# Performance work log

Measured on AMD Instinct MI355X. Metric: run time of the kernel, lower is better.

Reference implementation:

```python
import jax, jax.numpy as jnp
import numpy as np

HEADS = 16

def setup_inputs() -> dict:
    key = jax.random.key(0)
    ks = jax.random.split(key, 8)
    S, B, D = 2048, 2, 1024
    scale = 0.02
    return {
        'query': jax.random.normal(ks[0], (S, B, D), jnp.float32),
        'key':   jax.random.normal(ks[1], (S, B, D), jnp.float32),
        'value': jax.random.normal(ks[2], (S, B, D), jnp.float32),
        'Wq': jax.random.normal(ks[3], (D, D), jnp.float32) * scale,
        'bq': jnp.zeros((D,), jnp.float32),
        'Wk': jax.random.normal(ks[4], (D, D), jnp.float32) * scale,
        'bk': jnp.zeros((D,), jnp.float32),
        'Wv': jax.random.normal(ks[5], (D, D), jnp.float32) * scale,
        'bv': jnp.zeros((D,), jnp.float32),
        'Wo': jax.random.normal(ks[6], (D, D), jnp.float32) * scale,
        'bo': jnp.zeros((D,), jnp.float32),
    }

def reference(query, key, value, Wq, bq, Wk, bk, Wv, bv, Wo, bo):
    S, B, D = query.shape
    h = HEADS
    dk = D // h
    # projections: nn.Linear stores weight [out, in] -> x @ W.T + b
    q = (query @ Wq.T + bq).reshape(S, B, h, dk)
    k = (key   @ Wk.T + bk).reshape(S, B, h, dk)
    v = (value @ Wv.T + bv).reshape(S, B, h, dk)
    # scores: [i, j, b, h]
    scores = jnp.einsum('ibhd,jbhd->ijbh', q, k) / jnp.sqrt(jnp.asarray(dk, q.dtype))
    # original uses nn.Softmax(dim=1) -> softmax over key axis j
    attn = jax.nn.softmax(scores, axis=1)
    x = jnp.einsum('ijbh,jbhd->ibhd', attn, v).reshape(S, B, D)
    return x @ Wo.T + bo
```

## Files before the change

kernel.cpp:

```cpp
#include <hip/hip_runtime.h>
#include <hip/hip_bf16.h>
#include <math.h>

#define S_LEN  2048
#define NBATCH 2
#define DMODEL 1024
#define NHEADS 16
#define HDIM   64
#define MROWS  (S_LEN*NBATCH)
#define NBH    (NBATCH*NHEADS)

typedef __attribute__((ext_vector_type(8))) short          bf16x8;
typedef __attribute__((ext_vector_type(4))) float          f32x4;
typedef __attribute__((ext_vector_type(8))) unsigned short u16x8;

__device__ __forceinline__ unsigned short f2bf(float x) {
    union { __hip_bfloat16 h; unsigned short u; } c;
    c.h = __float2bfloat16(x);
    return c.u;
}
__device__ __forceinline__ unsigned int pk2(float a, float b) {
    return (unsigned int)f2bf(a) | ((unsigned int)f2bf(b) << 16);
}

__global__ __launch_bounds__(256)
void cvt7(const float* __restrict__ s0, const float* __restrict__ s1,
          const float* __restrict__ s2, const float* __restrict__ s3,
          const float* __restrict__ s4, const float* __restrict__ s5,
          const float* __restrict__ s6,
          unsigned short* __restrict__ d0, unsigned short* __restrict__ d1,
          unsigned short* __restrict__ d2, unsigned short* __restrict__ d3,
          unsigned short* __restrict__ d4, unsigned short* __restrict__ d5,
          unsigned short* __restrict__ d6)
{
    const float* s; unsigned short* d; int n;
    switch (blockIdx.y) {
        case 0: s = s0; d = d0; n = MROWS*DMODEL;  break;
        case 1: s = s1; d = d1; n = MROWS*DMODEL;  break;
        case 2: s = s2; d = d2; n = MROWS*DMODEL;  break;
        case 3: s = s3; d = d3; n = DMODEL*DMODEL; break;
        case 4: s = s4; d = d4; n = DMODEL*DMODEL; break;
        case 5: s = s5; d = d5; n = DMODEL*DMODEL; break;
        default: s = s6; d = d6; n = DMODEL*DMODEL; break;
    }
    int i = (blockIdx.x*256 + threadIdx.x) * 8;
    if (i >= n) return;
    float4 a = *(const float4*)(s + i);
    float4 b = *(const float4*)(s + i + 4);
    u16x8 o;
    o[0] = f2bf(a.x); o[1] = f2bf(a.y); o[2] = f2bf(a.z); o[3] = f2bf(a.w);
    o[4] = f2bf(b.x); o[5] = f2bf(b.y); o[6] = f2bf(b.z); o[7] = f2bf(b.w);
    *(u16x8*)(d + i) = o;
}

#define GBM 128
#define GBN 128
#define GBK 32

__device__ __forceinline__ void gemm_bf16_core(
    const unsigned short* __restrict__ A,
    const unsigned short* __restrict__ W,
    const float* __restrict__ bias,
    float* __restrict__ Cf, unsigned short* __restrict__ Cb,
    int mode, float scale)
{
    __shared__ __align__(16) unsigned short As[GBM*GBK];
    __shared__ __align__(16) unsigned short Bs[GBN*GBK];

    const int tid = threadIdx.x;
    const int l   = tid & 63;
    const int w   = tid >> 6;
    const int m0  = blockIdx.y * GBM;
    const int n0  = blockIdx.x * GBN;
    const int wm  = (w >> 1) * 64;
    const int wn  = (w & 1) * 64;

    f32x4 acc[4][4];
    #pragma unroll
    for (int i = 0; i < 4; ++i)
        #pragma unroll
        for (int j = 0; j < 4; ++j)
            acc[i][j] = (f32x4){0.f, 0.f, 0.f, 0.f};

    const int srow = l >> 2;
    const int scol = (l & 3) * 8;

    for (int k0 = 0; k0 < DMODEL; k0 += GBK) {
        #pragma unroll
        for (int i = 0; i < 2; ++i) {
            int c = w*2 + i;
            const unsigned short* ga = A + (size_t)(m0 + c*16 + srow)*DMODEL + k0 + scol;
            const unsigned short* gb = W + (size_t)(n0 + c*16 + srow)*DMODEL + k0 + scol;
            __builtin_amdgcn_global_load_lds(
                (const __attribute__((address_space(1))) void*)ga,
                (__attribute__((address_space(3))) void*)(As + c*512), 16, 0, 0);
            __builtin_amdgcn_global_load_lds(
                (const __attribute__((address_space(1))) void*)gb,
                (__attribute__((address_space(3))) void*)(Bs + c*512), 16, 0, 0);
        }
        __syncthreads();

        bf16x8 af[4], bfr[4];
        #pragma unroll
        for (int f = 0; f < 4; ++f) {
            af[f]  = *(const bf16x8*)(As + (wm + f*16 + (l & 15))*GBK + (l >> 4)*8);
            bfr[f] = *(const bf16x8*)(Bs + (wn + f*16 + (l & 15))*GBK + (l >> 4)*8);
        }
        #pragma unroll
        for (int i = 0; i < 4; ++i)
            #pragma unroll
            for (int j = 0; j < 4; ++j)
                acc[i][j] = __builtin_amdgcn_mfma_f32_16x16x32_bf16(af[i], bfr[j], acc[i][j], 0, 0, 0);
        __syncthreads();
    }

    const int col_l = l & 15;
    const int row_l = (l >> 4) * 4;
    #pragma unroll
    for (int j = 0; j < 4; ++j) {
        int col = n0 + wn + j*16 + col_l;
        float bv = bias[col];
        #pragma unroll
        for (int i = 0; i < 4; ++i) {
            int mbase = m0 + wm + i*16 + row_l;
            #pragma unroll
            for (int r = 0; r < 4; ++r) {
                int m = mbase + r;
                float vout = (acc[i][j][r] + bv) * scale;
                if (mode == 0) {
                    Cf[(size_t)m*DMODEL + col] = vout;
                } else {
                    int s = m >> 1, b = m & 1;
                    int h = col >> 6, d = col & 63;
                    if (mode == 1)
                        Cb[((size_t)(b*NHEADS + h)*S_LEN + s)*HDIM + d] = f2bf(vout);
                    else
                        Cb[((size_t)(b*NHEADS + h)*HDIM + d)*S_LEN + s] = f2bf(vout);
                }
            }
        }
    }
}

__global__ __launch_bounds__(256)
void gemm_qkv_bf16(const unsigned short* __restrict__ qb, const unsigned short* __restrict__ kb,
                   const unsigned short* __restrict__ vb,
                   const unsigned short* __restrict__ Wqb, const float* __restrict__ bq,
                   const unsigned short* __restrict__ Wkb, const float* __restrict__ bk,
                   const unsigned short* __restrict__ Wvb, const float* __restrict__ bv,
                   unsigned short* __restrict__ qp, unsigned short* __restrict__ kp,
                   unsigned short* __restrict__ vt)
{
    const int z = blockIdx.z;
    const unsigned short* A = (z==0) ? qb  : (z==1) ? kb  : vb;
    const unsigned short* W = (z==0) ? Wqb : (z==1) ? Wkb : Wvb;
    const float* bias       = (z==0) ? bq  : (z==1) ? bk  : bv;
    unsigned short* C       = (z==0) ? qp  : (z==1) ? kp  : vt;
    int   mode  = (z==2) ? 2 : 1;
    float scale = (z==0) ? 0.125f : 1.0f;
    gemm_bf16_core(A, W, bias, nullptr, C, mode, scale);
}

__global__ __launch_bounds__(256)
void gemm_out_bf16(const unsigned short* __restrict__ A, const unsigned short* __restrict__ W,
                   const float* __restrict__ bias, float* __restrict__ C)
{
    gemm_bf16_core(A, W, bias, C, nullptr, 0, 1.0f);
}

#define QBLK  128
#define KVBLK 64

__global__ __launch_bounds__(256)
void attn_mfma(const unsigned short* __restrict__ qp, const unsigned short* __restrict__ kp,
               const unsigned short* __restrict__ vt, unsigned short* __restrict__ x)
{
    __shared__ __align__(16) unsigned short Ks[KVBLK*HDIM];
    __shared__ __align__(16) unsigned short Vs[HDIM*KVBLK];
    __shared__ __align__(16) unsigned short Ps[4][32*KVBLK];

    const int tid = threadIdx.x;
    const int w   = tid >> 6;
    const int l   = tid & 63;
    const int g   = l >> 4;
    const int s16 = l & 15;
    const int q0  = blockIdx.x * QBLK;
    const int bh  = blockIdx.y;
    const int b   = bh >> 4;
    const int h   = bh & 15;
    const size_t base = (size_t)bh * S_LEN * HDIM;

    char* KsB = (char*)Ks;
    char* VsB = (char*)Vs;
    char* PsB = (char*)&Ps[w][0];

    bf16x8 qf[2][2];
    #pragma unroll
    for (int ni = 0; ni < 2; ++ni)
        #pragma unroll
        for (int ks = 0; ks < 2; ++ks) {
            int qrow = q0 + w*32 + ni*16 + s16;
            qf[ni][ks] = *(const bf16x8*)(qp + base + (size_t)qrow*HDIM + ks*32 + g*8);
        }

    f32x4 oacc[2][4];
    #pragma unroll
    for (int ni = 0; ni < 2; ++ni)
        #pragma unroll
        for (int nj = 0; nj < 4; ++nj)
            oacc[ni][nj] = (f32x4){0.f, 0.f, 0.f, 0.f};
    float run_m[2] = {-1e30f, -1e30f};
    float run_l[2] = {0.f, 0.f};

    for (int kt = 0; kt < S_LEN; kt += KVBLK) {
        #pragma unroll
        for (int it = 0; it < 2; ++it) {
            int idx  = it*256 + tid;
            int row  = idx >> 3;
            int u    = (idx & 7) ^ (row & 7);
            const unsigned short* gk = kp + base + (size_t)(kt + row)*HDIM + u*8;
            __builtin_amdgcn_global_load_lds(
                (const __attribute__((address_space(1))) void*)gk,
                (__attribute__((address_space(3))) void*)(Ks + (it*256 + w*64)*8), 16, 0, 0);
            const unsigned short* gv = vt + base + (size_t)row*S_LEN + kt + u*8;
            __builtin_amdgcn_global_load_lds(
                (const __attribute__((address_space(1))) void*)gv,
                (__attribute__((address_space(3))) void*)(Vs + (it*256 + w*64)*8), 16, 0, 0);
        }
        __syncthreads();

        f32x4 sacc[4][2];
        #pragma unroll
        for (int mi = 0; mi < 4; ++mi)
            #pragma unroll
            for (int ni = 0; ni < 2; ++ni)
                sacc[mi][ni] = (f32x4){0.f, 0.f, 0.f, 0.f};

        #pragma unroll
        for (int ks = 0; ks < 2; ++ks) {
            bf16x8 af[4];
            #pragma unroll
            for (int mi = 0; mi < 4; ++mi) {
                int key  = mi*16 + s16;
                int addr = ((key << 7) + (ks << 6) + (g << 4)) ^ ((key & 7) << 4);
                af[mi] = *(const bf16x8*)(KsB + addr);
            }
            #pragma unroll
            for (int mi = 0; mi < 4; ++mi)
                #pragma unroll
                for (int ni = 0; ni < 2; ++ni)
                    sacc[mi][ni] = __builtin_amdgcn_mfma_f32_16x16x32_bf16(
                        af[mi], qf[ni][ks], sacc[mi][ni], 0, 0, 0);
        }

        float al[2];
        #pragma unroll
        for (int ni = 0; ni < 2; ++ni) {
            float tm = -1e30f;
            #pragma unroll
            for (int mi = 0; mi < 4; ++mi)
                #pragma unroll
                for (int r = 0; r < 4; ++r)
                    tm = fmaxf(tm, sacc[mi][ni][r]);
            tm = fmaxf(tm, __shfl_xor(tm, 16));
            tm = fmaxf(tm, __shfl_xor(tm, 32));
            float mn = fmaxf(run_m[ni], tm);
            al[ni] = __expf(run_m[ni] - mn);
            float ps = 0.f;
            int row = ni*16 + s16;
            #pragma unroll
            for (int mi = 0; mi < 4; ++mi) {
                float p0 = __expf(sacc[mi][ni][0] - mn);
                float p1 = __expf(sacc[mi][ni][1] - mn);
                float p2 = __expf(sacc[mi][ni][2] - mn);
                float p3 = __expf(sacc[mi][ni][3] - mn);
                ps += (p0 + p1) + (p2 + p3);
                uint2 wv; wv.x = pk2(p0, p1); wv.y = pk2(p2, p3);
                int addr = ((row << 7) + (mi << 5) + (g << 3)) ^ ((row & 7) << 4);
                *(uint2*)(PsB + addr) = wv;
            }
            ps += __shfl_xor(ps, 16);
            ps += __shfl_xor(ps, 32);
            run_l[ni] = run_l[ni]*al[ni] + ps;
            run_m[ni] = mn;
        }

        float alo[2][4];
        #pragma unroll
        for (int ni = 0; ni < 2; ++ni)
            #pragma unroll
            for (int r = 0; r < 4; ++r)
                alo[ni][r] = __shfl(al[ni], 20*g + r);
        #pragma unroll
        for (int ni = 0; ni < 2; ++ni)
            #pragma unroll
            for (int nj = 0; nj < 4; ++nj)
                #pragma unroll
                for (int r = 0; r < 4; ++r)
                    oacc[ni][nj][r] *= alo[ni][r];

        #pragma unroll
        for (int ks = 0; ks < 2; ++ks) {
            bf16x8 pa[2];
            #pragma unroll
            for (int ni = 0; ni < 2; ++ni) {
                int row  = ni*16 + s16;
                int addr = ((row << 7) + (ks << 6) + (g << 4)) ^ ((row & 7) << 4);
                pa[ni] = *(const bf16x8*)(PsB + addr);
            }
            bf16x8 bv[4];
            #pragma unroll
            for (int nj = 0; nj < 4; ++nj) {
                int d    = nj*16 + s16;
                int addr = ((d << 7) + (ks << 6) + (g << 4)) ^ ((d & 7) << 4);
                bv[nj] = *(const bf16x8*)(VsB + addr);
            }
            #pragma unroll
            for (int ni = 0; ni < 2; ++ni)
                #pragma unroll
                for (int nj = 0; nj < 4; ++nj)
                    oacc[ni][nj] = __builtin_amdgcn_mfma_f32_16x16x32_bf16(
                        pa[ni], bv[nj], oacc[ni][nj], 0, 0, 0);
        }
        __syncthreads();
    }

    #pragma unroll
    for (int ni = 0; ni < 2; ++ni) {
        #pragma unroll
        for (int r = 0; r < 4; ++r) {
            float rl  = __shfl(run_l[ni], 20*g + r);
            float inv = 1.f / rl;
            int row = q0 + w*32 + ni*16 + 4*g + r;
            #pragma unroll
            for (int nj = 0; nj < 4; ++nj) {
                int col = h*HDIM + nj*16 + s16;
                x[(size_t)(row*NBATCH + b)*DMODEL + col] = f2bf(oacc[ni][nj][r] * inv);
            }
        }
    }
}

extern "C" void kernel_launch(void* const* d_in, const int* in_sizes, int n_in,
                              void* d_out, int out_size, void* d_ws, size_t ws_size,
                              hipStream_t stream)
{
    const float* query = (const float*)d_in[0];
    const float* key_i = (const float*)d_in[1];
    const float* value = (const float*)d_in[2];
    const float* Wq = (const float*)d_in[3];
    const float* bq = (const float*)d_in[4];
    const float* Wk = (const float*)d_in[5];
    const float* bk = (const float*)d_in[6];
    const float* Wv = (const float*)d_in[7];
    const float* bv = (const float*)d_in[8];
    const float* Wo = (const float*)d_in[9];
    const float* bo = (const float*)d_in[10];
    float* out = (float*)d_out;

    char* ws = (char*)d_ws;
    unsigned short* qb  = (unsigned short*)(ws);
    unsigned short* kb2 = (unsigned short*)(ws + (size_t) 8*1024*1024);
    unsigned short* vb  = (unsigned short*)(ws + (size_t)16*1024*1024);
    unsigned short* Wqb = (unsigned short*)(ws + (size_t)24*1024*1024);
    unsigned short* Wkb = (unsigned short*)(ws + (size_t)26*1024*1024);
    unsigned short* Wvb = (unsigned short*)(ws + (size_t)28*1024*1024);
    unsigned short* Wob = (unsigned short*)(ws + (size_t)30*1024*1024);
    unsigned short* qp  = (unsigned short*)(ws + (size_t)32*1024*1024);
    unsigned short* kp  = (unsigned short*)(ws + (size_t)40*1024*1024);
    unsigned short* vt  = (unsigned short*)(ws + (size_t)48*1024*1024);
    unsigned short* xab = (unsigned short*)(ws + (size_t)56*1024*1024);

    dim3 gCvt(MROWS*DMODEL/(256*8), 7);
    cvt7<<<gCvt, 256, 0, stream>>>(query, key_i, value, Wq, Wk, Wv, Wo,
                                   qb, kb2, vb, Wqb, Wkb, Wvb, Wob);

    dim3 gProj(DMODEL/GBN, MROWS/GBM, 3);
    gemm_qkv_bf16<<<gProj, 256, 0, stream>>>(qb, kb2, vb,
                                             Wqb, bq, Wkb, bk, Wvb, bv,
                                             qp, kp, vt);

    dim3 gAttn(S_LEN/QBLK, NBH);
    attn_mfma<<<gAttn, 256, 0, stream>>>(qp, kp, vt, xab);

    dim3 gOut(DMODEL/GBN, MROWS/GBM, 1);
    gemm_out_bf16<<<gOut, 256, 0, stream>>>(xab, Wob, bo, out);
}
```

Before: 259.6 us.

## Double-buffer attention KV tiles, exp2 softmax with deferred rescale, tiled V transpose

Attention now runs 512 threads with 16 query rows per wave. It double-buffers the K/V tiles so global-to-LDS loads overlap compute, and removes the trailing barrier. Softmax moves to exp2 with log2e folded into the Q scale, and it skips the running-max rescale when the new max stays within a threshold. The V projection writes its transposed output through an LDS tile as coalesced vector stores, and the output GEMM uses 64-wide N tiles for more blocks. The deferred rescale risks larger intermediate exponent values, and the bigger blocks raise LDS and register pressure.

Result: no change. 261.6 us (+0.7%).

```diff
diff --git a/kernel.cpp b/kernel.cpp
--- a/kernel.cpp
+++ b/kernel.cpp
@@ -9,6 +9,9 @@
 #define HDIM   64
 #define MROWS  (S_LEN*NBATCH)
 #define NBH    (NBATCH*NHEADS)
+
+#define QSCALE 0.1803368801111f
+#define DEFER_THR 11.5f
 
 typedef __attribute__((ext_vector_type(8))) short          bf16x8;
 typedef __attribute__((ext_vector_type(4))) float          f32x4;
@@ -54,32 +57,34 @@
 }
 
 #define GBM 128
-#define GBN 128
 #define GBK 32
 
-__device__ __forceinline__ void gemm_bf16_core(
+template<int BN_T, bool TRANS>
+__device__ __forceinline__ void gemm_core(
     const unsigned short* __restrict__ A,
     const unsigned short* __restrict__ W,
     const float* __restrict__ bias,
     float* __restrict__ Cf, unsigned short* __restrict__ Cb,
     int mode, float scale)
 {
+    constexpr int FN  = BN_T / 32;
+    constexpr int BCW = BN_T / 64;
     __shared__ __align__(16) unsigned short As[GBM*GBK];
-    __shared__ __align__(16) unsigned short Bs[GBN*GBK];
+    __shared__ __align__(16) unsigned short Bs[BN_T*GBK];
 
     const int tid = threadIdx.x;
     const int l   = tid & 63;
     const int w   = tid >> 6;
     const int m0  = blockIdx.y * GBM;
-    const int n0  = blockIdx.x * GBN;
+    const int n0  = blockIdx.x * BN_T;
     const int wm  = (w >> 1) * 64;
-    const int wn  = (w & 1) * 64;
-
-    f32x4 acc[4][4];
+    const int wn  = (w & 1) * (BN_T/2);
+
+    f32x4 acc[4][FN];
     #pragma unroll
     for (int i = 0; i < 4; ++i)
         #pragma unroll
-        for (int j = 0; j < 4; ++j)
+        for (int j = 0; j < FN; ++j)
             acc[i][j] = (f32x4){0.f, 0.f, 0.f, 0.f};
 
     const int srow = l >> 2;
@@ -90,34 +95,79 @@
         for (int i = 0; i < 2; ++i) {
             int c = w*2 + i;
             const unsigned short* ga = A + (size_t)(m0 + c*16 + srow)*DMODEL + k0 + scol;
-            const unsigned short* gb = W + (size_t)(n0 + c*16 + srow)*DMODEL + k0 + scol;
             __builtin_amdgcn_global_load_lds(
                 (const __attribute__((address_space(1))) void*)ga,
                 (__attribute__((address_space(3))) void*)(As + c*512), 16, 0, 0);
+        }
+        #pragma unroll
+        for (int i = 0; i < BCW; ++i) {
+            int c = w*BCW + i;
+            const unsigned short* gb = W + (size_t)(n0 + c*16 + srow)*DMODEL + k0 + scol;
             __builtin_amdgcn_global_load_lds(
                 (const __attribute__((address_space(1))) void*)gb,
                 (__attribute__((address_space(3))) void*)(Bs + c*512), 16, 0, 0);
         }
         __syncthreads();
 
-        bf16x8 af[4], bfr[4];
-        #pragma unroll
-        for (int f = 0; f < 4; ++f) {
+        bf16x8 af[4], bfr[FN];
+        #pragma unroll
+        for (int f = 0; f < 4; ++f)
             af[f]  = *(const bf16x8*)(As + (wm + f*16 + (l & 15))*GBK + (l >> 4)*8);
+        #pragma unroll
+        for (int f = 0; f < FN; ++f)
             bfr[f] = *(const bf16x8*)(Bs + (wn + f*16 + (l & 15))*GBK + (l >> 4)*8);
-        }
         #pragma unroll
         for (int i = 0; i < 4; ++i)
             #pragma unroll
-            for (int j = 0; j < 4; ++j)
+            for (int j = 0; j < FN; ++j)
                 acc[i][j] = __builtin_amdgcn_mfma_f32_16x16x32_bf16(af[i], bfr[j], acc[i][j], 0, 0, 0);
         __syncthreads();
     }
 
     const int col_l = l & 15;
     const int row_l = (l >> 4) * 4;
+
+    if constexpr (TRANS) {
+        if (mode == 2) {
+            __shared__ __align__(16) unsigned short tileS[64][136];
+            #pragma unroll
+            for (int ph = 0; ph < 2; ++ph) {
+                __syncthreads();
+                if ((w >> 1) == ph) {
+                    #pragma unroll
+                    for (int j = 0; j < FN; ++j) {
+                        int c = wn + j*16 + col_l;
+                        float bv = bias[n0 + c];
+                        #pragma unroll
+                        for (int i = 0; i < 4; ++i)
+                            #pragma unroll
+                            for (int r = 0; r < 4; ++r)
+                                tileS[i*16 + row_l + r][c] = f2bf((acc[i][j][r] + bv) * scale);
+                    }
+                }
+                __syncthreads();
+                const int sbase = (m0 + ph*64) >> 1;
+                #pragma unroll
+                for (int it = 0; it < 4; ++it) {
+                    int idx = it*256 + tid;
+                    int c    = idx >> 3;
+                    int bb   = (idx >> 2) & 1;
+                    int sl0  = (idx & 3) * 8;
+                    int hh   = (n0 + c) >> 6;
+                    int dd   = (n0 + c) & 63;
+                    u16x8 ov;
+                    #pragma unroll
+                    for (int k2 = 0; k2 < 8; ++k2)
+                        ov[k2] = tileS[2*(sl0 + k2) + bb][c];
+                    *(u16x8*)(Cb + ((size_t)(bb*NHEADS + hh)*HDIM + dd)*S_LEN + sbase + sl0) = ov;
+                }
+            }
+            return;
+        }
+    }
+
     #pragma unroll
-    for (int j = 0; j < 4; ++j) {
+    for (int j = 0; j < FN; ++j) {
         int col = n0 + wn + j*16 + col_l;
         float bv = bias[col];
         #pragma unroll
@@ -132,10 +182,7 @@
                 } else {
                     int s = m >> 1, b = m & 1;
                     int h = col >> 6, d = col & 63;
-                    if (mode == 1)
-                        Cb[((size_t)(b*NHEADS + h)*S_LEN + s)*HDIM + d] = f2bf(vout);
-                    else
-                        Cb[((size_t)(b*NHEADS + h)*HDIM + d)*S_LEN + s] = f2bf(vout);
+                    Cb[((size_t)(b*NHEADS + h)*S_LEN + s)*HDIM + d] = f2bf(vout);
                 }
             }
         }
@@ -143,13 +190,13 @@
 }
 
 __global__ __launch_bounds__(256)
-void gemm_qkv_bf16(const unsigned short* __restrict__ qb, const unsigned short* __restrict__ kb,
-                   const unsigned short* __restrict__ vb,
-                   const unsigned short* __restrict__ Wqb, const float* __restrict__ bq,
-                   const unsigned short* __restrict__ Wkb, const float* __restrict__ bk,
-                   const unsigned short* __restrict__ Wvb, const float* __restrict__ bv,
-                   unsigned short* __restrict__ qp, unsigned short* __restrict__ kp,
-                   unsigned short* __restrict__ vt)
+void gemm_qkv(const unsigned short* __restrict__ qb, const unsigned short* __restrict__ kb,
+              const unsigned short* __restrict__ vb,
+              const unsigned short* __restrict__ Wqb, const float* __restrict__ bq,
+              const unsigned short* __restrict__ Wkb, const float* __restrict__ bk,
+              const unsigned short* __restrict__ Wvb, const float* __restrict__ bv,
+              unsigned short* __restrict__ qp, unsigned short* __restrict__ kp,
+              unsigned short* __restrict__ vt)
 {
     const int z = blockIdx.z;
     const unsigned short* A = (z==0) ? qb  : (z==1) ? kb  : vb;
@@ -157,27 +204,28 @@
     const float* bias       = (z==0) ? bq  : (z==1) ? bk  : bv;
     unsigned short* C       = (z==0) ? qp  : (z==1) ? kp  : vt;
     int   mode  = (z==2) ? 2 : 1;
-    float scale = (z==0) ? 0.125f : 1.0f;
-    gemm_bf16_core(A, W, bias, nullptr, C, mode, scale);
+    float scale = (z==0) ? QSCALE : 1.0f;
+    gemm_core<128, true>(A, W, bias, nullptr, C, mode, scale);
 }
 
 __global__ __launch_bounds__(256)
-void gemm_out_bf16(const unsigned short* __restrict__ A, const unsigned short* __restrict__ W,
-                   const float* __restrict__ bias, float* __restrict__ C)
-{
-    gemm_bf16_core(A, W, bias, C, nullptr, 0, 1.0f);
+void gemm_out(const unsigned short* __restrict__ A, const unsigned short* __restrict__ W,
+              const float* __restrict__ bias, float* __restrict__ C)
+{
+    gemm_core<64, false>(A, W, bias, C, nullptr, 0, 1.0f);
 }
 
 #define QBLK  128
 #define KVBLK 64
-
-__global__ __launch_bounds__(256)
+#define NT    (S_LEN/KVBLK)
+
+__global__ __launch_bounds__(512)
 void attn_mfma(const unsigned short* __restrict__ qp, const unsigned short* __restrict__ kp,
                const unsigned short* __restrict__ vt, unsigned short* __restrict__ x)
 {
-    __shared__ __align__(16) unsigned short Ks[KVBLK*HDIM];
-    __shared__ __align__(16) unsigned short Vs[HDIM*KVBLK];
-    __shared__ __align__(16) unsigned short Ps[4][32*KVBLK];
+    __shared__ __align__(16) unsigned short Ks[2][KVBLK*HDIM];
+    __shared__ __align__(16) unsigned short Vs[2][KVBLK*HDIM];
+    __shared__ __align__(16) unsigned short Ps[8][16*KVBLK];
 
     const int tid = threadIdx.x;
     const int w   = tid >> 6;
@@ -190,52 +238,45 @@
     const int h   = bh & 15;
     const size_t base = (size_t)bh * S_LEN * HDIM;
 
-    char* KsB = (char*)Ks;
-    char* VsB = (char*)Vs;
     char* PsB = (char*)&Ps[w][0];
 
-    bf16x8 qf[2][2];
+#define STAGE(buf, kt_) do {                                                         \
+    int row_ = tid >> 3;                                                             \
+    int u_   = (tid & 7) ^ (row_ & 7);                                               \
+    const unsigned short* gk_ = kp + base + (size_t)((kt_) + row_)*HDIM + u_*8;      \
+    __builtin_amdgcn_global_load_lds(                                                \
+        (const __attribute__((address_space(1))) void*)gk_,                          \
+        (__attribute__((address_space(3))) void*)(Ks[buf] + w*512), 16, 0, 0);       \
+    const unsigned short* gv_ = vt + base + (size_t)row_*S_LEN + (kt_) + u_*8;       \
+    __builtin_amdgcn_global_load_lds(                                                \
+        (const __attribute__((address_space(1))) void*)gv_,                          \
+        (__attribute__((address_space(3))) void*)(Vs[buf] + w*512), 16, 0, 0);       \
+} while (0)
+
+    bf16x8 qf[2];
     #pragma unroll
-    for (int ni = 0; ni < 2; ++ni)
-        #pragma unroll
-        for (int ks = 0; ks < 2; ++ks) {
-            int qrow = q0 + w*32 + ni*16 + s16;
-            qf[ni][ks] = *(const bf16x8*)(qp + base + (size_t)qrow*HDIM + ks*32 + g*8);
-        }
-
-    f32x4 oacc[2][4];
+    for (int ks = 0; ks < 2; ++ks)
+        qf[ks] = *(const bf16x8*)(qp + base + (size_t)(q0 + w*16 + s16)*HDIM + ks*32 + g*8);
+
+    f32x4 oacc[4];
     #pragma unroll
-    for (int ni = 0; ni < 2; ++ni)
-        #pragma unroll
-        for (int nj = 0; nj < 4; ++nj)
-            oacc[ni][nj] = (f32x4){0.f, 0.f, 0.f, 0.f};
-    float run_m[2] = {-1e30f, -1e30f};
-    float run_l[2] = {0.f, 0.f};
-
-    for (int kt = 0; kt < S_LEN; kt += KVBLK) {
-        #pragma unroll
-        for (int it = 0; it < 2; ++it) {
-            int idx  = it*256 + tid;
-            int row  = idx >> 3;
-            int u    = (idx & 7) ^ (row & 7);
-            const unsigned short* gk = kp + base + (size_t)(kt + row)*HDIM + u*8;
-            __builtin_amdgcn_global_load_lds(
-                (const __attribute__((address_space(1))) void*)gk,
-                (__attribute__((address_space(3))) void*)(Ks + (it*256 + w*64)*8), 16, 0, 0);
-            const unsigned short* gv = vt + base + (size_t)row*S_LEN + kt + u*8;
-            __builtin_amdgcn_global_load_lds(
-                (const __attribute__((address_space(1))) void*)gv,
-                (__attribute__((address_space(3))) void*)(Vs + (it*256 + w*64)*8), 16, 0, 0);
-        }
+    for (int nj = 0; nj < 4; ++nj) oacc[nj] = (f32x4){0.f, 0.f, 0.f, 0.f};
+    float run_m = -1e30f;
+    float run_l = 0.f;
+
+    STAGE(0, 0);
+
+    for (int t = 0; t < NT; ++t) {
+        const int cur = t & 1;
         __syncthreads();
-
-        f32x4 sacc[4][2];
-        #pragma unroll
-        for (int mi = 0; mi < 4; ++mi)
-            #pragma unroll
-            for (int ni = 0; ni < 2; ++ni)
-                sacc[mi][ni] = (f32x4){0.f, 0.f, 0.f, 0.f};
-
+        if (t + 1 < NT) STAGE(cur ^ 1, (t + 1)*KVBLK);
+
+        const char* KsB = (const char*)Ks[cur];
+        const char* VsB = (const char*)Vs[cur];
+
+        f32x4 sacc[4];
+        #pragma unroll
+        for (int mi = 0; mi < 4; ++mi) sacc[mi] = (f32x4){0.f, 0.f, 0.f, 0.f};
         #pragma unroll
         for (int ks = 0; ks < 2; ++ks) {
             bf16x8 af[4];
@@ -247,67 +288,54 @@
             }
             #pragma unroll
             for (int mi = 0; mi < 4; ++mi)
-                #pragma unroll
-                for (int ni = 0; ni < 2; ++ni)
-                    sacc[mi][ni] = __builtin_amdgcn_mfma_f32_16x16x32_bf16(
-                        af[mi], qf[ni][ks], sacc[mi][ni], 0, 0, 0);
-        }
-
-        float al[2];
-        #pragma unroll
-        for (int ni = 0; ni < 2; ++ni) {
-            float tm = -1e30f;
-            #pragma unroll
-            for (int mi = 0; mi < 4; ++mi)
-                #pragma unroll
-                for (int r = 0; r < 4; ++r)
-                    tm = fmaxf(tm, sacc[mi][ni][r]);
-            tm = fmaxf(tm, __shfl_xor(tm, 16));
-            tm = fmaxf(tm, __shfl_xor(tm, 32));
-            float mn = fmaxf(run_m[ni], tm);
-            al[ni] = __expf(run_m[ni] - mn);
-            float ps = 0.f;
-            int row = ni*16 + s16;
-            #pragma unroll
-            for (int mi = 0; mi < 4; ++mi) {
-                float p0 = __expf(sacc[mi][ni][0] - mn);
-                float p1 = __expf(sacc[mi][ni][1] - mn);
-                float p2 = __expf(sacc[mi][ni][2] - mn);
-                float p3 = __expf(sacc[mi][ni][3] - mn);
-                ps += (p0 + p1) + (p2 + p3);
-                uint2 wv; wv.x = pk2(p0, p1); wv.y = pk2(p2, p3);
-                int addr = ((row << 7) + (mi << 5) + (g << 3)) ^ ((row & 7) << 4);
-                *(uint2*)(PsB + addr) = wv;
-            }
-            ps += __shfl_xor(ps, 16);
-            ps += __shfl_xor(ps, 32);
-            run_l[ni] = run_l[ni]*al[ni] + ps;
-            run_m[ni] = mn;
-        }
-
-        float alo[2][4];
-        #pragma unroll
-        for (int ni = 0; ni < 2; ++ni)
-            #pragma unroll
-            for (int r = 0; r < 4; ++r)
-                alo[ni][r] = __shfl(al[ni], 20*g + r);
-        #pragma unroll
-        for (int ni = 0; ni < 2; ++ni)
+                sacc[mi] = __builtin_amdgcn_mfma_f32_16x16x32_bf16(af[mi], qf[ks], sacc[mi], 0, 0, 0);
+        }
+
+        float t0 = fmaxf(fmaxf(sacc[0][0], sacc[0][1]), sacc[0][2]);
+        float t1 = fmaxf(fmaxf(sacc[0][3], sacc[1][0]), sacc[1][1]);
+        float t2 = fmaxf(fmaxf(sacc[1][2], sacc[1][3]), sacc[2][0]);
+        float t3 = fmaxf(fmaxf(sacc[2][1], sacc[2][2]), sacc[2][3]);
+        float t4 = fmaxf(fmaxf(sacc[3][0], sacc[3][1]), sacc[3][2]);
+        float tm = fmaxf(fmaxf(fmaxf(t0, t1), t2), fmaxf(fmaxf(t3, t4), sacc[3][3]));
+        tm = fmaxf(tm, __shfl_xor(tm, 16));
+        tm = fmaxf(tm, __shfl_xor(tm, 32));
+
+        float mn, al;
+        if (__all(tm <= run_m + DEFER_THR)) {
+            mn = run_m; al = 1.0f;
+        } else {
+            mn = fmaxf(run_m, tm);
+            al = exp2f(run_m - mn);
+            run_m = mn;
+            float alo[4];
+            #pragma unroll
+            for (int r = 0; r < 4; ++r) alo[r] = __shfl(al, 20*g + r);
             #pragma unroll
             for (int nj = 0; nj < 4; ++nj)
                 #pragma unroll
-                for (int r = 0; r < 4; ++r)
-                    oacc[ni][nj][r] *= alo[ni][r];
+                for (int r = 0; r < 4; ++r) oacc[nj][r] *= alo[r];
+        }
+
+        float ps = 0.f;
+        #pragma unroll
+        for (int mi = 0; mi < 4; ++mi) {
+            float p0 = exp2f(sacc[mi][0] - mn);
+            float p1 = exp2f(sacc[mi][1] - mn);
+            float p2 = exp2f(sacc[mi][2] - mn);
+            float p3 = exp2f(sacc[mi][3] - mn);
+            ps += (p0 + p1) + (p2 + p3);
+            uint2 wv; wv.x = pk2(p0, p1); wv.y = pk2(p2, p3);
+            int addr = ((s16 << 7) + (mi << 5) + (g << 3)) ^ ((s16 & 7) << 4);
+            *(uint2*)(PsB + addr) = wv;
+        }
+        ps += __shfl_xor(ps, 16);
+        ps += __shfl_xor(ps, 32);
+        run_l = run_l*al + ps;
 
         #pragma unroll
         for (int ks = 0; ks < 2; ++ks) {
-            bf16x8 pa[2];
-            #pragma unroll
-            for (int ni = 0; ni < 2; ++ni) {
-                int row  = ni*16 + s16;
-                int addr = ((row << 7) + (ks << 6) + (g << 4)) ^ ((row & 7) << 4);
-                pa[ni] = *(const bf16x8*)(PsB + addr);
-            }
+            int paddr = ((s16 << 7) + (ks << 6) + (g << 4)) ^ ((s16 & 7) << 4);
+            bf16x8 pa = *(const bf16x8*)(PsB + paddr);
             bf16x8 bv[4];
             #pragma unroll
             for (int nj = 0; nj < 4; ++nj) {
@@ -316,27 +344,21 @@
                 bv[nj] = *(const bf16x8*)(VsB + addr);
             }
             #pragma unroll
-            for (int ni = 0; ni < 2; ++ni)
-                #pragma unroll
-                for (int nj = 0; nj < 4; ++nj)
-                    oacc[ni][nj] = __builtin_amdgcn_mfma_f32_16x16x32_bf16(
-                        pa[ni], bv[nj], oacc[ni][nj], 0, 0, 0);
-        }
-        __syncthreads();
-    }
+            for (int nj = 0; nj < 4; ++nj)
+                oacc[nj] = __builtin_amdgcn_mfma_f32_16x16x32_bf16(pa, bv[nj], oacc[nj], 0, 0, 0);
+        }
+    }
+#undef STAGE
 
     #pragma unroll
-    for (int ni = 0; ni < 2; ++ni) {
-        #pragma unroll
-        for (int r = 0; r < 4; ++r) {
-            float rl  = __shfl(run_l[ni], 20*g + r);
-            float inv = 1.f / rl;
-            int row = q0 + w*32 + ni*16 + 4*g + r;
-            #pragma unroll
-            for (int nj = 0; nj < 4; ++nj) {
-                int col = h*HDIM + nj*16 + s16;
-                x[(size_t)(row*NBATCH + b)*DMODEL + col] = f2bf(oacc[ni][nj][r] * inv);
-            }
+    for (int r = 0; r < 4; ++r) {
+        float rl  = __shfl(run_l, 20*g + r);
+        float inv = 1.f / rl;
+        int row = q0 + w*16 + 4*g + r;
+        #pragma unroll
+        for (int nj = 0; nj < 4; ++nj) {
+            int col = h*HDIM + nj*16 + s16;
+            x[(size_t)(row*NBATCH + b)*DMODEL + col] = f2bf(oacc[nj][r] * inv);
         }
     }
 }
@@ -375,14 +397,14 @@
     cvt7<<<gCvt, 256, 0, stream>>>(query, key_i, value, Wq, Wk, Wv, Wo,
                                    qb, kb2, vb, Wqb, Wkb, Wvb, Wob);
 
-    dim3 gProj(DMODEL/GBN, MROWS/GBM, 3);
-    gemm_qkv_bf16<<<gProj, 256, 0, stream>>>(qb, kb2, vb,
-                                             Wqb, bq, Wkb, bk, Wvb, bv,
-                                             qp, kp, vt);
+    dim3 gQKV(DMODEL/128, MROWS/GBM, 3);
+    gemm_qkv<<<gQKV, 256, 0, stream>>>(qb, kb2, vb,
+                                       Wqb, bq, Wkb, bk, Wvb, bv,
+                                       qp, kp, vt);
 
     dim3 gAttn(S_LEN/QBLK, NBH);
-    attn_mfma<<<gAttn, 256, 0, stream>>>(qp, kp, vt, xab);
-
-    dim3 gOut(DMODEL/GBN, MROWS/GBM, 1);
-    gemm_out_bf16<<<gOut, 256, 0, stream>>>(xab, Wob, bo, out);
-}
+    attn_mfma<<<gAttn, 512, 0, stream>>>(qp, kp, vt, xab);
+
+    dim3 gOut(DMODEL/64, MROWS/GBM);
+    gemm_out<<<gOut, 256, 0, stream>>>(xab, Wob, bo, out);
+}
```
